# Optimization experiments

Measured on AMD Instinct MI355X. Metric: run time of the kernel, lower is better.

## Reference

```python
import jax, jax.numpy as jnp
import numpy as np

WS = (7, 7)          # window size
DIM = 256            # projection_dim
HEADS = 8
B = 2048             # batch * num_windows
NW = 64              # windows per image (mask leading dim)


def _relative_position_index(ws):
    coords = np.stack(np.meshgrid(np.arange(ws[0]), np.arange(ws[1]), indexing='ij'))  # [2,h,w]
    flat = coords.reshape(2, -1)                                   # [2, h*w]
    rel = flat[:, :, None] - flat[:, None, :]                      # [2, N, N]
    rel = rel.transpose(1, 2, 0)                                   # [N, N, 2]
    rel[:, :, 0] += ws[0] - 1
    rel[:, :, 1] += ws[1] - 1
    idx = rel[:, :, 0] * (2 * ws[1] - 1) + rel[:, :, 1]            # [N, N]
    return idx.reshape(-1).astype(np.int32)                        # [N*N]


def setup_inputs() -> dict:
    key = jax.random.key(0)
    ks = jax.random.split(key, 6)
    N = WS[0] * WS[1]
    return {
        'x': jax.random.normal(ks[0], (B, N, DIM), jnp.float32),
        'mask': jax.random.normal(ks[1], (NW, N, N), jnp.float32),  # additive shift mask
        'qkv_w': jax.random.normal(ks[2], (DIM, 3 * DIM), jnp.float32) * (DIM ** -0.5),
        'qkv_b': jnp.zeros((3 * DIM,), jnp.float32),
        'proj_w': jax.random.normal(ks[3], (DIM, DIM), jnp.float32) * (DIM ** -0.5),
        'proj_b': jnp.zeros((DIM,), jnp.float32),
        'bias_table': jax.random.normal(ks[4], ((2 * WS[0] - 1) * (2 * WS[1] - 1), HEADS), jnp.float32) * 0.02,
        'rel_index': jnp.asarray(_relative_position_index(WS)),
    }


def reference(x, mask, qkv_w, qkv_b, proj_w, proj_b, bias_table, rel_index):
    Bn, N, C = x.shape
    hd = C // HEADS
    scale = hd ** -0.5
    qkv = x @ qkv_w + qkv_b                               # [B, N, 3C]
    qkv = qkv.reshape(Bn, N, 3, HEADS, hd).transpose(2, 0, 3, 1, 4)  # [3, B, H, N, hd]
    q, k, v = qkv[0], qkv[1], qkv[2]
    attn = jnp.einsum('bhnd,bhmd->bhnm', q * scale, k)    # [B, H, N, N]
    # gathered relative position bias: [N*N, H] -> [H, N, N]
    bias = bias_table[rel_index].reshape(N, N, HEADS).transpose(2, 0, 1)
    attn = attn + bias[None]
    nW = mask.shape[0]
    attn = attn.reshape(Bn // nW, nW, HEADS, N, N) + mask[None, :, None]
    attn = attn.reshape(Bn, HEADS, N, N)
    attn = jax.nn.softmax(attn, axis=-1)
    out = jnp.einsum('bhnm,bhmd->bhnd', attn, v)          # [B, H, N, hd]
    out = out.transpose(0, 2, 1, 3).reshape(Bn, N, C)
    return out @ proj_w + proj_b
```

## Files before the change

kernel.cpp:

```cpp
#include <hip/hip_runtime.h>


typedef __attribute__((ext_vector_type(8))) short v8s;
typedef __attribute__((ext_vector_type(4))) float v4f;

__device__ __forceinline__ unsigned short f2bf(float f) {
    union { float f; unsigned int i; } v; v.f = f;
    unsigned int x = v.i;
    return (unsigned short)((x + 0x7fffu + ((x >> 16) & 1u)) >> 16);
}

#define NW1 196608
#define NW2 65536
#define NB1 768
#define NCB 1605632
#define QSCALE_LOG2E 0.25503487f
#define LOG2E 1.4426950408889634f

__global__ void wattn_preproc(const float* __restrict__ qkv_w,
                              const float* __restrict__ qkv_b,
                              const float* __restrict__ proj_w,
                              const float* __restrict__ bias_table,
                              const float* __restrict__ mask,
                              const int* __restrict__ rel_index,
                              unsigned short* __restrict__ W1f,
                              unsigned short* __restrict__ W2f,
                              float* __restrict__ B1v,
                              float* __restrict__ CBf)
{
    const int idx = blockIdx.x * 256 + threadIdx.x;
    if (idx < NW1) {
        const int j = idx & 7, l = (idx >> 3) & 63, s = (idx >> 9) & 7, T = idx >> 12;
        const int k = s * 32 + (l >> 4) * 8 + j;
        const int n = T * 16 + (l & 15);
        const int hh = n / 96, sub = n % 96;
        const int col = (sub < 32) ? (hh * 32 + sub)
                      : (sub < 64) ? (256 + hh * 32 + (sub - 32))
                                   : (512 + hh * 32 + (sub - 64));
        float v = qkv_w[k * 768 + col];
        if (sub < 32) v *= QSCALE_LOG2E;
        W1f[idx] = f2bf(v);
    } else if (idx < NW1 + NW2) {
        const int t = idx - NW1;
        const int j = t & 7, l = (t >> 3) & 63, s = (t >> 9) & 7, T = t >> 12;
        const int k = s * 32 + (l >> 4) * 8 + j;
        const int n = T * 16 + (l & 15);
        W2f[t] = f2bf(proj_w[k * 256 + n]);
    } else if (idx < NW1 + NW2 + NB1) {
        const int n = idx - NW1 - NW2;
        const int hh = n / 96, sub = n % 96;
        const int col = (sub < 32) ? (hh * 32 + sub)
                      : (sub < 64) ? (256 + hh * 32 + (sub - 32))
                                   : (512 + hh * 32 + (sub - 64));
        float v = qkv_b[col];
        if (sub < 32) v *= QSCALE_LOG2E;
        B1v[n] = v;
    } else {
        const int t = idx - (NW1 + NW2 + NB1);
        if (t < NCB) {
            const int c = t & 63;
            const int rr = t >> 6;
            const int r = rr % 49;
            const int q2 = rr / 49;
            const int hh = q2 & 7;
            const int w = q2 >> 3;
            float v;
            if (c < 49) {
                const int ri = rel_index[r * 49 + c];
                v = (bias_table[ri * 8 + hh] + mask[(w * 49 + r) * 49 + c]) * LOG2E;
            } else {
                v = -1e30f;
            }
            CBf[t] = v;
        }
    }
}

__global__ __launch_bounds__(256, 2)
void wattn_main(const float* __restrict__ x,
                const unsigned short* __restrict__ W1f,
                const float* __restrict__ B1v,
                const float* __restrict__ CB,
                const unsigned short* __restrict__ W2f,
                const float* __restrict__ proj_b,
                float* __restrict__ out)
{
    __shared__ __align__(16) unsigned short xs[49 * 136];
    __shared__ __align__(16) unsigned short qs[49 * 40];
    __shared__ __align__(16) unsigned short ks[49 * 40];
    __shared__ __align__(16) unsigned short Vs[32 * 72];
    __shared__ __align__(16) unsigned short Ps[49 * 72];
    __shared__ __align__(16) unsigned short Os[49 * 264];

    const int tid  = threadIdx.x;
    const int wave = tid >> 6;
    const int lane = tid & 63;
    const int quad = lane >> 4;
    const int l15  = lane & 15;
    const int b    = blockIdx.x;
    const int widx = b & 63;
    const float* xw = x + (long)b * 49 * 256;
    const v4f zero4 = {0.0f, 0.0f, 0.0f, 0.0f};

    for (int i = tid; i < 32 * 15; i += 256) { const int d = i / 15, c = 49 + i % 15; Vs[d * 72 + c] = 0; }

    int arow[4];
    #pragma unroll
    for (int mt = 0; mt < 4; ++mt) {
        int m = mt * 16 + l15; if (m > 48) m = 48;
        arow[mt] = m * 136 + quad * 8;
    }

    #pragma unroll 1
    for (int p = 0; p < 2; ++p) {
        v4f acc[6][4];
        #pragma unroll
        for (int i = 0; i < 6; ++i)
            #pragma unroll
            for (int mt = 0; mt < 4; ++mt) acc[i][mt] = zero4;

        const int T0 = p * 24 + wave * 6;
        const unsigned short* bb = W1f + T0 * 4096 + lane * 8;

        #pragma unroll 1
        for (int ch = 0; ch < 2; ++ch) {
            __syncthreads();
            for (int i = tid; i < 1568; i += 256) {
                const int r = i >> 5, cq = i & 31;
                const float4 v = *reinterpret_cast<const float4*>(xw + r * 256 + ch * 128 + cq * 4);
                ushort4 o;
                o.x = f2bf(v.x); o.y = f2bf(v.y); o.z = f2bf(v.z); o.w = f2bf(v.w);
                *reinterpret_cast<ushort4*>(&xs[r * 136 + cq * 4]) = o;
            }
            __syncthreads();
            #pragma unroll
            for (int s = 0; s < 4; ++s) {
                v8s afr[4];
                #pragma unroll
                for (int mt = 0; mt < 4; ++mt)
                    afr[mt] = *reinterpret_cast<const v8s*>(&xs[arow[mt] + s * 32]);
                v8s bfr[6];
                #pragma unroll
                for (int i = 0; i < 6; ++i)
                    bfr[i] = *reinterpret_cast<const v8s*>(bb + i * 4096 + (ch * 4 + s) * 512);
                #pragma unroll
                for (int i = 0; i < 6; ++i)
                    #pragma unroll
                    for (int mt = 0; mt < 4; ++mt)
                        acc[i][mt] = __builtin_amdgcn_mfma_f32_16x16x32_bf16(afr[mt], bfr[i], acc[i][mt], 0, 0, 0);
            }
        }
        #pragma unroll
        for (int i = 0; i < 6; ++i) {
            const float bv = B1v[(T0 + i) * 16 + l15];
            #pragma unroll
            for (int mt = 0; mt < 4; ++mt) {
                acc[i][mt].x += bv; acc[i][mt].y += bv; acc[i][mt].z += bv; acc[i][mt].w += bv;
            }
        }

        for (int hh = 0; hh < 4; ++hh) {
            __syncthreads();
            if (wave == hh) {
                #pragma unroll
                for (int i = 0; i < 6; ++i) {
                    #pragma unroll
                    for (int mt = 0; mt < 4; ++mt) {
                        const int m0 = mt * 16 + quad * 4;
                        float vv[4] = {acc[i][mt].x, acc[i][mt].y, acc[i][mt].z, acc[i][mt].w};
                        if (i < 2) {
                            const int c = i * 16 + l15;
                            #pragma unroll
                            for (int r = 0; r < 4; ++r)
                                if (m0 + r < 49) qs[(m0 + r) * 40 + c] = f2bf(vv[r]);
                        } else if (i < 4) {
                            const int c = (i - 2) * 16 + l15;
                            #pragma unroll
                            for (int r = 0; r < 4; ++r)
                                if (m0 + r < 49) ks[(m0 + r) * 40 + c] = f2bf(vv[r]);
                        } else {
                            const int d = (i - 4) * 16 + l15;
                            if (mt < 3) {
                                ushort4 pk;
                                pk.x = f2bf(vv[0]); pk.y = f2bf(vv[1]);
                                pk.z = f2bf(vv[2]); pk.w = f2bf(vv[3]);
                                *reinterpret_cast<ushort4*>(&Vs[d * 72 + m0]) = pk;
                            } else if (quad == 0) {
                                Vs[d * 72 + 48] = f2bf(vv[0]);
                            }
                        }
                    }
                }
            }
            __syncthreads();

            const int h = p * 4 + hh;

            int aqr = wave * 16 + l15; if (aqr > 48) aqr = 48;
            const v8s aq = *reinterpret_cast<const v8s*>(&qs[aqr * 40 + quad * 8]);
            v4f sacc[4];
            #pragma unroll
            for (int nt = 0; nt < 4; ++nt) {
                int bkr = nt * 16 + l15; if (bkr > 48) bkr = 48;
                const v8s bk = *reinterpret_cast<const v8s*>(&ks[bkr * 40 + quad * 8]);
                sacc[nt] = __builtin_amdgcn_mfma_f32_16x16x32_bf16(aq, bk, zero4, 0, 0, 0);
            }

            const float* cbb = CB + (((long)widx * 8 + h) * 49) * 64;
            float pout[4][4];
            #pragma unroll
            for (int r = 0; r < 4; ++r) {
                const int m = wave * 16 + quad * 4 + r;
                const int mc = m > 48 ? 48 : m;
                float s0 = sacc[0][r] + cbb[mc * 64 + l15];
                float s1 = sacc[1][r] + cbb[mc * 64 + 16 + l15];
                float s2 = sacc[2][r] + cbb[mc * 64 + 32 + l15];
                float s3 = sacc[3][r] + cbb[mc * 64 + 48 + l15];
                float mx = fmaxf(fmaxf(s0, s1), fmaxf(s2, s3));
                #pragma unroll
                for (int off = 1; off < 16; off <<= 1) mx = fmaxf(mx, __shfl_xor(mx, off, 16));
                const float e0 = __builtin_exp2f(s0 - mx);
                const float e1 = __builtin_exp2f(s1 - mx);
                const float e2 = __builtin_exp2f(s2 - mx);
                const float e3 = __builtin_exp2f(s3 - mx);
                float sm = (e0 + e1) + (e2 + e3);
                #pragma unroll
                for (int off = 1; off < 16; off <<= 1) sm += __shfl_xor(sm, off, 16);
                const float rs = __builtin_amdgcn_rcpf(sm);
                pout[r][0] = e0 * rs; pout[r][1] = e1 * rs;
                pout[r][2] = e2 * rs; pout[r][3] = e3 * rs;
            }
            #pragma unroll
            for (int r = 0; r < 4; ++r) {
                const int m = wave * 16 + quad * 4 + r;
                if (m < 49) {
                    #pragma unroll
                    for (int nt = 0; nt < 4; ++nt)
                        Ps[m * 72 + nt * 16 + l15] = f2bf(pout[r][nt]);
                }
            }
            __syncthreads();

            int mrc = wave * 16 + l15; if (mrc > 48) mrc = 48;
            v4f oacc[2] = {zero4, zero4};
            #pragma unroll
            for (int kt = 0; kt < 2; ++kt) {
                const v8s ap = *reinterpret_cast<const v8s*>(&Ps[mrc * 72 + kt * 32 + quad * 8]);
                #pragma unroll
                for (int n2 = 0; n2 < 2; ++n2) {
                    const v8s bv = *reinterpret_cast<const v8s*>(&Vs[(n2 * 16 + l15) * 72 + kt * 32 + quad * 8]);
                    oacc[n2] = __builtin_amdgcn_mfma_f32_16x16x32_bf16(ap, bv, oacc[n2], 0, 0, 0);
                }
            }
            #pragma unroll
            for (int n2 = 0; n2 < 2; ++n2) {
                const int c = h * 32 + n2 * 16 + l15;
                #pragma unroll
                for (int r = 0; r < 4; ++r) {
                    const int m = wave * 16 + quad * 4 + r;
                    if (m < 49) Os[m * 264 + c] = f2bf(oacc[n2][r]);
                }
            }
        }
    }

    __syncthreads();

    v4f pacc[4][4];
    #pragma unroll
    for (int i = 0; i < 4; ++i)
        #pragma unroll
        for (int mt = 0; mt < 4; ++mt) pacc[i][mt] = zero4;

    int orow[4];
    #pragma unroll
    for (int mt = 0; mt < 4; ++mt) {
        int m = mt * 16 + l15; if (m > 48) m = 48;
        orow[mt] = m * 264 + quad * 8;
    }
    const unsigned short* wb = W2f + (wave * 4) * 4096 + lane * 8;

    #pragma unroll
    for (int s = 0; s < 8; ++s) {
        v8s afr[4];
        #pragma unroll
        for (int mt = 0; mt < 4; ++mt)
            afr[mt] = *reinterpret_cast<const v8s*>(&Os[orow[mt] + s * 32]);
        #pragma unroll
        for (int i = 0; i < 4; ++i) {
            const v8s bfp = *reinterpret_cast<const v8s*>(wb + i * 4096 + s * 512);
            #pragma unroll
            for (int mt = 0; mt < 4; ++mt)
                pacc[i][mt] = __builtin_amdgcn_mfma_f32_16x16x32_bf16(afr[mt], bfp, pacc[i][mt], 0, 0, 0);
        }
    }

    #pragma unroll
    for (int i = 0; i < 4; ++i) {
        const int c = (wave * 4 + i) * 16 + l15;
        const float pb = proj_b[c];
        #pragma unroll
        for (int mt = 0; mt < 4; ++mt) {
            #pragma unroll
            for (int r = 0; r < 4; ++r) {
                const int m = mt * 16 + quad * 4 + r;
                if (m < 49) out[((long)b * 49 + m) * 256 + c] = pacc[i][mt][r] + pb;
            }
        }
    }
}

extern "C" void kernel_launch(void* const* d_in, const int* in_sizes, int n_in,
                              void* d_out, int out_size, void* d_ws, size_t ws_size,
                              hipStream_t stream)
{
    const float* x          = (const float*)d_in[0];
    const float* mask       = (const float*)d_in[1];
    const float* qkv_w      = (const float*)d_in[2];
    const float* qkv_b      = (const float*)d_in[3];
    const float* proj_w     = (const float*)d_in[4];
    const float* proj_b     = (const float*)d_in[5];
    const float* bias_table = (const float*)d_in[6];
    const int*   rel_index  = (const int*)d_in[7];
    float* out = (float*)d_out;

    char* ws = (char*)d_ws;
    unsigned short* W1f = (unsigned short*)(ws);
    unsigned short* W2f = (unsigned short*)(ws + 393216);
    float*          B1v = (float*)(ws + 524288);
    float*          CBf = (float*)(ws + 527360);

    wattn_preproc<<<7299, 256, 0, stream>>>(qkv_w, qkv_b, proj_w, bias_table, mask,
                                            rel_index, W1f, W2f, B1v, CBf);
    wattn_main<<<2048, 256, 0, stream>>>(x, W1f, B1v, CBf, W2f, proj_b, out);
}
```

Baseline: 365.3 us.

## Give each wave its own head with private LDS region, removing block barriers

```diff
diff --git a/kernel.cpp b/kernel.cpp
--- a/kernel.cpp
+++ b/kernel.cpp
@@ -85,11 +85,8 @@
                 const float* __restrict__ proj_b,
                 float* __restrict__ out)
 {
-    __shared__ __align__(16) unsigned short xs[49 * 136];
-    __shared__ __align__(16) unsigned short qs[49 * 40];
-    __shared__ __align__(16) unsigned short ks[49 * 40];
-    __shared__ __align__(16) unsigned short Vs[32 * 72];
-    __shared__ __align__(16) unsigned short Ps[49 * 72];
+    __shared__ __align__(16) unsigned short xs[49 * 72];
+    __shared__ __align__(16) unsigned short wreg[4][5832];
     __shared__ __align__(16) unsigned short Os[49 * 264];
 
     const int tid  = threadIdx.x;
@@ -101,14 +98,13 @@
     const int widx = b & 63;
     const float* xw = x + (long)b * 49 * 256;
     const v4f zero4 = {0.0f, 0.0f, 0.0f, 0.0f};
-
-    for (int i = tid; i < 32 * 15; i += 256) { const int d = i / 15, c = 49 + i % 15; Vs[d * 72 + c] = 0; }
+    unsigned short* Wr = wreg[wave];
 
     int arow[4];
     #pragma unroll
     for (int mt = 0; mt < 4; ++mt) {
         int m = mt * 16 + l15; if (m > 48) m = 48;
-        arow[mt] = m * 136 + quad * 8;
+        arow[mt] = m * 72 + quad * 8;
     }
 
     #pragma unroll 1
@@ -123,18 +119,18 @@
         const unsigned short* bb = W1f + T0 * 4096 + lane * 8;
 
         #pragma unroll 1
-        for (int ch = 0; ch < 2; ++ch) {
+        for (int ch = 0; ch < 4; ++ch) {
             __syncthreads();
-            for (int i = tid; i < 1568; i += 256) {
-                const int r = i >> 5, cq = i & 31;
-                const float4 v = *reinterpret_cast<const float4*>(xw + r * 256 + ch * 128 + cq * 4);
+            for (int i = tid; i < 784; i += 256) {
+                const int r = i >> 4, cq = i & 15;
+                const float4 v = *reinterpret_cast<const float4*>(xw + r * 256 + ch * 64 + cq * 4);
                 ushort4 o;
                 o.x = f2bf(v.x); o.y = f2bf(v.y); o.z = f2bf(v.z); o.w = f2bf(v.w);
-                *reinterpret_cast<ushort4*>(&xs[r * 136 + cq * 4]) = o;
+                *reinterpret_cast<ushort4*>(&xs[r * 72 + cq * 4]) = o;
             }
             __syncthreads();
             #pragma unroll
-            for (int s = 0; s < 4; ++s) {
+            for (int s = 0; s < 2; ++s) {
                 v8s afr[4];
                 #pragma unroll
                 for (int mt = 0; mt < 4; ++mt)
@@ -142,7 +138,7 @@
                 v8s bfr[6];
                 #pragma unroll
                 for (int i = 0; i < 6; ++i)
-                    bfr[i] = *reinterpret_cast<const v8s*>(bb + i * 4096 + (ch * 4 + s) * 512);
+                    bfr[i] = *reinterpret_cast<const v8s*>(bb + i * 4096 + (ch * 2 + s) * 512);
                 #pragma unroll
                 for (int i = 0; i < 6; ++i)
                     #pragma unroll
@@ -159,63 +155,47 @@
             }
         }
 
-        for (int hh = 0; hh < 4; ++hh) {
-            __syncthreads();
-            if (wave == hh) {
-                #pragma unroll
-                for (int i = 0; i < 6; ++i) {
-                    #pragma unroll
-                    for (int mt = 0; mt < 4; ++mt) {
-                        const int m0 = mt * 16 + quad * 4;
-                        float vv[4] = {acc[i][mt].x, acc[i][mt].y, acc[i][mt].z, acc[i][mt].w};
-                        if (i < 2) {
-                            const int c = i * 16 + l15;
-                            #pragma unroll
-                            for (int r = 0; r < 4; ++r)
-                                if (m0 + r < 49) qs[(m0 + r) * 40 + c] = f2bf(vv[r]);
-                        } else if (i < 4) {
-                            const int c = (i - 2) * 16 + l15;
-                            #pragma unroll
-                            for (int r = 0; r < 4; ++r)
-                                if (m0 + r < 49) ks[(m0 + r) * 40 + c] = f2bf(vv[r]);
-                        } else {
-                            const int d = (i - 4) * 16 + l15;
-                            if (mt < 3) {
-                                ushort4 pk;
-                                pk.x = f2bf(vv[0]); pk.y = f2bf(vv[1]);
-                                pk.z = f2bf(vv[2]); pk.w = f2bf(vv[3]);
-                                *reinterpret_cast<ushort4*>(&Vs[d * 72 + m0]) = pk;
-                            } else if (quad == 0) {
-                                Vs[d * 72 + 48] = f2bf(vv[0]);
-                            }
-                        }
-                    }
-                }
-            }
-            __syncthreads();
-
-            const int h = p * 4 + hh;
-
-            int aqr = wave * 16 + l15; if (aqr > 48) aqr = 48;
-            const v8s aq = *reinterpret_cast<const v8s*>(&qs[aqr * 40 + quad * 8]);
-            v4f sacc[4];
-            #pragma unroll
-            for (int nt = 0; nt < 4; ++nt) {
-                int bkr = nt * 16 + l15; if (bkr > 48) bkr = 48;
-                const v8s bk = *reinterpret_cast<const v8s*>(&ks[bkr * 40 + quad * 8]);
-                sacc[nt] = __builtin_amdgcn_mfma_f32_16x16x32_bf16(aq, bk, zero4, 0, 0, 0);
-            }
-
-            const float* cbb = CB + (((long)widx * 8 + h) * 49) * 64;
+        const int h = p * 4 + wave;
+
+        #pragma unroll
+        for (int i = 0; i < 4; ++i) {
+            const int base = (i < 2) ? 0 : 1960;
+            const int c = (i & 1) * 16 + l15;
+            #pragma unroll
+            for (int mt = 0; mt < 4; ++mt) {
+                const int m0 = mt * 16 + quad * 4;
+                #pragma unroll
+                for (int r = 0; r < 4; ++r)
+                    if (m0 + r < 49) Wr[base + (m0 + r) * 40 + c] = f2bf(acc[i][mt][r]);
+            }
+        }
+
+        v8s aq[4], bk[4];
+        #pragma unroll
+        for (int t = 0; t < 4; ++t) {
+            int rq = t * 16 + l15; if (rq > 48) rq = 48;
+            aq[t] = *reinterpret_cast<const v8s*>(&Wr[rq * 40 + quad * 8]);
+            bk[t] = *reinterpret_cast<const v8s*>(&Wr[1960 + rq * 40 + quad * 8]);
+        }
+        v4f sacc[4][4];
+        #pragma unroll
+        for (int mt = 0; mt < 4; ++mt)
+            #pragma unroll
+            for (int nt = 0; nt < 4; ++nt)
+                sacc[mt][nt] = __builtin_amdgcn_mfma_f32_16x16x32_bf16(aq[mt], bk[nt], zero4, 0, 0, 0);
+
+        const float* cbb = CB + ((long)widx * 8 + h) * 49 * 64;
+        #pragma unroll
+        for (int mt = 0; mt < 4; ++mt) {
             float pout[4][4];
             #pragma unroll
             for (int r = 0; r < 4; ++r) {
-                const int m = wave * 16 + quad * 4 + r;
+                const int m = mt * 16 + quad * 4 + r;
                 const int mc = m > 48 ? 48 : m;
-                float s0 = sacc[0][r] + cbb[mc * 64 + l15];
-                float s1 = sacc[1][r] + cbb[mc * 64 + 16 + l15];
-                float s2 = sacc[2][r] + cbb[mc * 64 + 32 + l15];
-                float s3 = sacc[3][r] + cbb[mc * 64 + 48 + l15];
+                float s0 = sacc[mt][0][r] + cbb[mc * 64 + l15];
+                float s1 = sacc[mt][1][r] + cbb[mc * 64 + 16 + l15];
+                float s2 = sacc[mt][2][r] + cbb[mc * 64 + 32 + l15];
+                float s3 = sacc[mt][3][r] + cbb[mc * 64 + 48 + l15];
                 float mx = fmaxf(fmaxf(s0, s1), fmaxf(s2, s3));
                 #pragma unroll
                 for (int off = 1; off < 16; off <<= 1) mx = fmaxf(mx, __shfl_xor(mx, off, 16));
@@ -232,32 +212,61 @@
             }
             #pragma unroll
             for (int r = 0; r < 4; ++r) {
-                const int m = wave * 16 + quad * 4 + r;
+                const int m = mt * 16 + quad * 4 + r;
                 if (m < 49) {
                     #pragma unroll
                     for (int nt = 0; nt < 4; ++nt)
-                        Ps[m * 72 + nt * 16 + l15] = f2bf(pout[r][nt]);
+                        Wr[m * 72 + nt * 16 + l15] = f2bf(pout[r][nt]);
                 }
             }
-            __syncthreads();
-
-            int mrc = wave * 16 + l15; if (mrc > 48) mrc = 48;
+        }
+
+        #pragma unroll
+        for (int i = 4; i < 6; ++i) {
+            const int d = (i - 4) * 16 + l15;
+            #pragma unroll
+            for (int mt = 0; mt < 4; ++mt) {
+                const int m0 = mt * 16 + quad * 4;
+                if (mt < 3) {
+                    ushort4 pk;
+                    pk.x = f2bf(acc[i][mt][0]); pk.y = f2bf(acc[i][mt][1]);
+                    pk.z = f2bf(acc[i][mt][2]); pk.w = f2bf(acc[i][mt][3]);
+                    *reinterpret_cast<ushort4*>(&Wr[3528 + d * 72 + m0]) = pk;
+                } else if (quad == 0) {
+                    Wr[3528 + d * 72 + 48] = f2bf(acc[i][mt][0]);
+                }
+            }
+        }
+        {
+            const int d  = lane >> 1;
+            const int c0 = 49 + (lane & 1) * 8;
+            const int ce = (lane & 1) ? 64 : 57;
+            for (int c = c0; c < ce; ++c) Wr[3528 + d * 72 + c] = 0;
+        }
+
+        v8s bv2[2][2];
+        #pragma unroll
+        for (int n2 = 0; n2 < 2; ++n2)
+            #pragma unroll
+            for (int kt = 0; kt < 2; ++kt)
+                bv2[n2][kt] = *reinterpret_cast<const v8s*>(&Wr[3528 + (n2 * 16 + l15) * 72 + kt * 32 + quad * 8]);
+        #pragma unroll
+        for (int mt = 0; mt < 4; ++mt) {
+            int mrc = mt * 16 + l15; if (mrc > 48) mrc = 48;
             v4f oacc[2] = {zero4, zero4};
             #pragma unroll
             for (int kt = 0; kt < 2; ++kt) {
-                const v8s ap = *reinterpret_cast<const v8s*>(&Ps[mrc * 72 + kt * 32 + quad * 8]);
-                #pragma unroll
-                for (int n2 = 0; n2 < 2; ++n2) {
-                    const v8s bv = *reinterpret_cast<const v8s*>(&Vs[(n2 * 16 + l15) * 72 + kt * 32 + quad * 8]);
-                    oacc[n2] = __builtin_amdgcn_mfma_f32_16x16x32_bf16(ap, bv, oacc[n2], 0, 0, 0);
-                }
+                const v8s ap = *reinterpret_cast<const v8s*>(&Wr[mrc * 72 + kt * 32 + quad * 8]);
+                #pragma unroll
+                for (int n2 = 0; n2 < 2; ++n2)
+                    oacc[n2] = __builtin_amdgcn_mfma_f32_16x16x32_bf16(ap, bv2[n2][kt], oacc[n2], 0, 0, 0);
             }
             #pragma unroll
             for (int n2 = 0; n2 < 2; ++n2) {
                 const int c = h * 32 + n2 * 16 + l15;
                 #pragma unroll
                 for (int r = 0; r < 4; ++r) {
-                    const int m = wave * 16 + quad * 4 + r;
+                    const int m = mt * 16 + quad * 4 + r;
                     if (m < 49) Os[m * 264 + c] = f2bf(oacc[n2][r]);
                 }
             }
```

Result: faster. 350.0 us (-4.2%).
